# Performance work log

Measured on AMD Instinct MI355X. Metric: run time of the kernel, lower is better.

Reference implementation:

```python
import jax, jax.numpy as jnp
import numpy as np
from jax import lax

B, C, H, W = 8, 1, 1024, 1024


def _conv5(x, w, b):
    # x: [N, Cin, Hs, Ws], w: [1, Cin, 5, 5], b: [1]; 'same' padding (pad=2)
    return lax.conv_general_dilated(
        x, w, window_strides=(1, 1), padding=((2, 2), (2, 2)),
        dimension_numbers=("NCHW", "OIHW", "NCHW")) + b[None, :, None, None]


def _dir_scan(seq, pw, pb, cw, cb):
    # seq: [T, B, 1, Hs, Ws] slices in processing order.
    # s_0 = preconv(seq[0]); s_t = conv(cat(s_{t-1}, seq[t])).
    s0 = _conv5(seq[0], pw, pb)

    def step(carry, sl):
        s = _conv5(jnp.concatenate([carry, sl], axis=1), cw, cb)
        return s, s

    _, ys = lax.scan(step, s0, seq[1:])
    return jnp.concatenate([s0[None], ys], axis=0)  # [T, B, 1, Hs, Ws]


def setup_inputs() -> dict:
    key = jax.random.key(0)
    ks = jax.random.split(key, 17)
    inp = {"x": jax.random.normal(ks[0], (B, C, H, W), jnp.float32)}
    for i, name in enumerate(["pre1", "pre2", "pre3", "pre4"]):
        inp[name + "_w"] = jax.random.normal(ks[1 + 2 * i], (1, 1, 5, 5), jnp.float32) * 0.2
        inp[name + "_b"] = jax.random.normal(ks[2 + 2 * i], (1,), jnp.float32) * 0.1
    for i, name in enumerate(["c1", "c2", "c3", "c4"]):
        inp[name + "_w"] = jax.random.normal(ks[9 + 2 * i], (1, 2, 5, 5), jnp.float32) * 0.2
        inp[name + "_b"] = jax.random.normal(ks[10 + 2 * i], (1,), jnp.float32) * 0.1
    return inp


def reference(x, pre1_w, pre1_b, pre2_w, pre2_b, pre3_w, pre3_b, pre4_w, pre4_b,
              c1_w, c1_b, c2_w, c2_b, c3_w, c3_b, c4_w, c4_b):
    # Pass 1: top->down scan over rows h; conv spatial plane is (C, W).
    seq1 = jnp.transpose(x, (2, 0, 1, 3))[:, :, None]        # [H, B, 1, C, W]
    s1 = _dir_scan(seq1, pre1_w, pre1_b, c1_w, c1_b)          # states s_0..s_{H-1}
    # Pass 2: torch reads out1 channels H-1..0, i.e. s_0..s_{H-1} in order.
    s2 = _dir_scan(s1, pre2_w, pre2_b, c2_w, c2_b)            # states u_0..u_{H-1}
    # out2 (torch layout): channel j holds u_{H-1-j} -> [B, H, C, W]
    out2 = jnp.transpose(s2[::-1, :, 0], (1, 0, 2, 3))
    # Pass 3: left->right scan over w; conv spatial plane is (H, C).
    seq3 = jnp.transpose(out2, (3, 0, 1, 2))[:, :, None]      # [W, B, 1, H, C]
    s3 = _dir_scan(seq3, pre3_w, pre3_b, c3_w, c3_b)          # states v_0..v_{W-1}
    # Pass 4: torch reads out3 channels W-1..0, i.e. v_0..v_{W-1} in order.
    s4 = _dir_scan(s3, pre4_w, pre4_b, c4_w, c4_b)            # states z_0..z_{W-1}
    out4 = jnp.transpose(s4[::-1, :, 0], (1, 0, 2, 3))        # [B, W, H, C]
    return jnp.transpose(out4, (0, 3, 2, 1))                  # [B, C, H, W]
```

## Files before the change

### kernel.cpp

```cpp
#include <hip/hip_runtime.h>

#define HW 1024
#define NB 8
#define LPT 16
#define CHUNK 4
#define NCH (HW / CHUNK)
#define WARM 64

__device__ __forceinline__ float shfl_up1(float v)  { return __shfl_up(v, 1, 64); }
__device__ __forceinline__ float shfl_dn1(float v)  { return __shfl_down(v, 1, 64); }


#define LOADX(XD, T)                                                        \
    {                                                                       \
        const int tr_ = ((T) < HW) ? (T) : (HW - 1);                        \
        const float* rp_ = Ib + (size_t)tr_ * HW + base;                    \
        *(float4*)&XD[2]  = ((const float4*)rp_)[0];                        \
        *(float4*)&XD[6]  = ((const float4*)rp_)[1];                        \
        *(float4*)&XD[10] = ((const float4*)rp_)[2];                        \
        *(float4*)&XD[14] = ((const float4*)rp_)[3];                        \
    }

#define STEP(IS_PRE2, T, XC, XN, SC, SN, UC, UN)                            \
    {                                                                       \
        const int t_ = (T);                                                 \
        LOADX(XN, t_ + 2);                                                  \
        _Pragma("unroll")                                                   \
        for (int i = 0; i < 16; ++i) {                                      \
            float acc = cB1;                                                \
            _Pragma("unroll")                                               \
            for (int k = 0; k < 5; ++k) acc += A1[k] * SC[i + k];           \
            _Pragma("unroll")                                               \
            for (int k = 0; k < 5; ++k) acc += B1[k] * XC[i + k];           \
            SN[2 + i] = acc;                                                \
        }                                                                   \
        if (IS_PRE2) {                                                      \
            _Pragma("unroll")                                               \
            for (int i = 0; i < 16; ++i) {                                  \
                float acc = pB2;                                            \
                _Pragma("unroll")                                           \
                for (int k = 0; k < 5; ++k) acc += P2[k] * SC[i + k];       \
                UN[2 + i] = acc;                                            \
            }                                                               \
        } else {                                                            \
            _Pragma("unroll")                                               \
            for (int i = 0; i < 16; ++i) {                                  \
                float acc = cB2;                                            \
                _Pragma("unroll")                                           \
                for (int k = 0; k < 5; ++k) acc += A2[k] * UC[i + k];       \
                _Pragma("unroll")                                           \
                for (int k = 0; k < 5; ++k) acc += B2[k] * SC[i + k];       \
                UN[2 + i] = acc;                                            \
            }                                                               \
        }                                                                   \
              \
        float sa_ = shfl_up1(SN[16]), sb_ = shfl_up1(SN[17]);               \
        float sc_ = shfl_dn1(SN[2]),  sd_ = shfl_dn1(SN[3]);                \
        float ua_ = shfl_up1(UN[16]), ub_ = shfl_up1(UN[17]);               \
        float uc_ = shfl_dn1(UN[2]),  ud_ = shfl_dn1(UN[3]);                \
        float xa_ = shfl_up1(XN[16]), xb_ = shfl_up1(XN[17]);               \
        float xc_ = shfl_dn1(XN[2]),  xd_ = shfl_dn1(XN[3]);                \
        if (t_ >= T0) {       \
            _Pragma("unroll")                                               \
            for (int q = 0; q < 4; ++q) {                                   \
                float4 v_;                                                  \
                v_.x = UN[2 + 4 * q]; v_.y = UN[3 + 4 * q];                 \
                v_.z = UN[4 + 4 * q]; v_.w = UN[5 + 4 * q];                 \
                *(float4*)(Ob + (size_t)t_ * HW + base + 4 * q) = v_;       \
            }                                                               \
        }                                                                   \
        SN[0]  = lo ? 0.f : sa_; SN[1]  = lo ? 0.f : sb_;                   \
        SN[18] = hi ? 0.f : sc_; SN[19] = hi ? 0.f : sd_;                   \
        UN[0]  = lo ? 0.f : ua_; UN[1]  = lo ? 0.f : ub_;                   \
        UN[18] = hi ? 0.f : uc_; UN[19] = hi ? 0.f : ud_;                   \
        XN[0]  = lo ? 0.f : xa_; XN[1]  = lo ? 0.f : xb_;                   \
        XN[18] = hi ? 0.f : xc_; XN[19] = hi ? 0.f : xd_;                   \
    }

__global__ __launch_bounds__(64, 2) void scan_pair_wave(
    const float* __restrict__ I, float* __restrict__ O,
    const float* __restrict__ pw1, const float* __restrict__ pb1,
    const float* __restrict__ pw2, const float* __restrict__ pb2,
    const float* __restrict__ cw1, const float* __restrict__ cb1,
    const float* __restrict__ cw2, const float* __restrict__ cb2,
    int toff, int tstr)
{
    const int b     = blockIdx.x;
    const int chunk = blockIdx.y;
    const int T0 = chunk * CHUNK, T1 = T0 + CHUNK;
    const int g0 = (T0 - WARM > 0) ? (T0 - WARM) : 0;

    const int lane = threadIdx.x;
    const int base = lane * LPT;
    const bool lo = (lane == 0), hi = (lane == 63);

    float P1[5], P2[5], A1[5], B1[5], A2[5], B2[5];
#pragma unroll
    for (int k = 0; k < 5; ++k) {
        P1[k] = pw1[toff + k * tstr];
        P2[k] = pw2[toff + k * tstr];
        A1[k] = cw1[toff + k * tstr];
        B1[k] = cw1[25 + toff + k * tstr];
        A2[k] = cw2[toff + k * tstr];
        B2[k] = cw2[25 + toff + k * tstr];
    }
    const float pB1 = pb1[0], pB2 = pb2[0], cB1 = cb1[0], cB2 = cb2[0];

    const float* Ib = I + (size_t)b * HW * HW;
    float*       Ob = O + (size_t)b * HW * HW;

    float xeA[20], xeB[20], seA[20], seB[20], ueA[20], ueB[20];

#pragma unroll
    for (int i = 0; i < 20; ++i) ueA[i] = 0.f;

    LOADX(xeB, g0);
    LOADX(xeA, g0 + 1);
    {
        float a0 = shfl_up1(xeB[16]), a1 = shfl_up1(xeB[17]);
        float a2 = shfl_dn1(xeB[2]),  a3 = shfl_dn1(xeB[3]);
        float b0 = shfl_up1(xeA[16]), b1 = shfl_up1(xeA[17]);
        float b2 = shfl_dn1(xeA[2]),  b3 = shfl_dn1(xeA[3]);
        xeB[0]  = lo ? 0.f : a0; xeB[1]  = lo ? 0.f : a1;
        xeB[18] = hi ? 0.f : a2; xeB[19] = hi ? 0.f : a3;
        xeA[0]  = lo ? 0.f : b0; xeA[1]  = lo ? 0.f : b1;
        xeA[18] = hi ? 0.f : b2; xeA[19] = hi ? 0.f : b3;
    }
    if (g0 == 0) {
#pragma unroll
        for (int i = 0; i < 16; ++i) {
            float acc = pB1;
#pragma unroll
            for (int k = 0; k < 5; ++k) acc += P1[k] * xeB[i + k];
            seA[2 + i] = acc;
        }
    } else {
#pragma unroll
        for (int i = 0; i < 16; ++i) {
            float acc = cB1;
#pragma unroll
            for (int k = 0; k < 5; ++k) acc += B1[k] * xeB[i + k];
            seA[2 + i] = acc;
        }
    }
    {
        float sa = shfl_up1(seA[16]), sb = shfl_up1(seA[17]);
        float sc = shfl_dn1(seA[2]),  sd = shfl_dn1(seA[3]);
        seA[0]  = lo ? 0.f : sa; seA[1]  = lo ? 0.f : sb;
        seA[18] = hi ? 0.f : sc; seA[19] = hi ? 0.f : sd;
    }

    if (g0 == 0) {
        STEP(1, 0, xeA, xeB, seA, seB, ueA, ueB);
        for (int t = 1; t + 1 <= T1 - 2; t += 2) {
            STEP(0, t,     xeB, xeA, seB, seA, ueB, ueA);
            STEP(0, t + 1, xeA, xeB, seA, seB, ueA, ueB);
        }
    } else {
        int t = g0;
        for (; t + 1 <= T1 - 2; t += 2) {
            STEP(0, t,     xeA, xeB, seA, seB, ueA, ueB);
            STEP(0, t + 1, xeB, xeA, seB, seA, ueB, ueA);
        }
        STEP(0, T1 - 2, xeA, xeB, seA, seB, ueA, ueB);
    }

    {
        float un[16];
#pragma unroll
        for (int i = 0; i < 16; ++i) {
            float acc = cB2;
#pragma unroll
            for (int k = 0; k < 5; ++k) acc += A2[k] * ueB[i + k];
#pragma unroll
            for (int k = 0; k < 5; ++k) acc += B2[k] * seB[i + k];
            un[i] = acc;
        }
#pragma unroll
        for (int q = 0; q < 4; ++q) {
            float4 v;
            v.x = un[4 * q + 0]; v.y = un[4 * q + 1];
            v.z = un[4 * q + 2]; v.w = un[4 * q + 3];
            *(float4*)(Ob + (size_t)(T1 - 1) * HW + base + 4 * q) = v;
        }
    }
}

__global__ void transposeR_kernel(const float* __restrict__ in, float* __restrict__ out)
{
    __shared__ float tile[32][33];
    const int b  = blockIdx.z;
    const int r0 = blockIdx.y * 32;
    const int c0 = blockIdx.x * 32;
    const int tx = threadIdx.x, ty = threadIdx.y;
    const float* inb  = in  + (size_t)b * HW * HW;
    float*       outb = out + (size_t)b * HW * HW;

#pragma unroll
    for (int i = ty; i < 32; i += 8)
        tile[i][tx] = inb[(size_t)(HW - 1 - (r0 + i)) * HW + c0 + tx];
    __syncthreads();
#pragma unroll
    for (int i = ty; i < 32; i += 8)
        outb[(size_t)(c0 + i) * HW + r0 + tx] = tile[tx][i];
}

extern "C" void kernel_launch(void* const* d_in, const int* in_sizes, int n_in,
                              void* d_out, int out_size, void* d_ws, size_t ws_size,
                              hipStream_t stream)
{
    const float* x      = (const float*)d_in[0];
    const float* pre1_w = (const float*)d_in[1];
    const float* pre1_b = (const float*)d_in[2];
    const float* pre2_w = (const float*)d_in[3];
    const float* pre2_b = (const float*)d_in[4];
    const float* pre3_w = (const float*)d_in[5];
    const float* pre3_b = (const float*)d_in[6];
    const float* pre4_w = (const float*)d_in[7];
    const float* pre4_b = (const float*)d_in[8];
    const float* c1_w   = (const float*)d_in[9];
    const float* c1_b   = (const float*)d_in[10];
    const float* c2_w   = (const float*)d_in[11];
    const float* c2_b   = (const float*)d_in[12];
    const float* c3_w   = (const float*)d_in[13];
    const float* c3_b   = (const float*)d_in[14];
    const float* c4_w   = (const float*)d_in[15];
    const float* c4_b   = (const float*)d_in[16];

    float* out = (float*)d_out;
    float* ws  = (float*)d_ws;

    dim3 sg(NB, NCH), sb(64);
    dim3 tg(32, 32, NB), tb(32, 8);

    scan_pair_wave<<<sg, sb, 0, stream>>>(
        x, ws, pre1_w, pre1_b, pre2_w, pre2_b, c1_w, c1_b, c2_w, c2_b, 10, 1);

    transposeR_kernel<<<tg, tb, 0, stream>>>(ws, out);

    scan_pair_wave<<<sg, sb, 0, stream>>>(
        out, ws, pre3_w, pre3_b, pre4_w, pre4_b, c3_w, c3_b, c4_w, c4_b, 2, 5);

    transposeR_kernel<<<tg, tb, 0, stream>>>(ws, out);
}
```

Measured before the change: 204.5 us.

## Load x halos directly from memory, double chunk size, hoist state shuffles

Each lane now reads its two-element left and right halo of the input row straight from global memory instead of exchanging it through cross-lane shuffles. The halo is patched in at the start of the next step, which takes the shuffles off the critical path. The state shuffles move to just after the state is computed so they overlap with the second conv. The time chunk per block doubles, which halves the redundant warm-up recomputation relative to useful work but also halves the number of blocks. Launch bounds drop to one block per SIMD, which allows more registers.

```diff
diff --git a/kernel.cpp b/kernel.cpp
--- a/kernel.cpp
+++ b/kernel.cpp
@@ -3,7 +3,7 @@
 #define HW 1024
 #define NB 8
 #define LPT 16
-#define CHUNK 4
+#define CHUNK 8
 #define NCH (HW / CHUNK)
 #define WARM 64
 
@@ -11,7 +11,7 @@
 __device__ __forceinline__ float shfl_dn1(float v)  { return __shfl_down(v, 1, 64); }
 
 
-#define LOADX(XD, T)                                                        \
+#define LOADX(XD, XL, XR, T)                                                \
     {                                                                       \
         const int tr_ = ((T) < HW) ? (T) : (HW - 1);                        \
         const float* rp_ = Ib + (size_t)tr_ * HW + base;                    \
@@ -19,12 +19,22 @@
         *(float4*)&XD[6]  = ((const float4*)rp_)[1];                        \
         *(float4*)&XD[10] = ((const float4*)rp_)[2];                        \
         *(float4*)&XD[14] = ((const float4*)rp_)[3];                        \
-    }
-
-#define STEP(IS_PRE2, T, XC, XN, SC, SN, UC, UN)                            \
+        XL = *(const float2*)(lo ? rp_ : rp_ - 2);          \
+        XR = *(const float2*)(hi ? rp_ : rp_ + 16);        \
+    }
+
+#define FINX(XC, XL, XR)                                                    \
+    {                                                                       \
+        XC[0]  = lo ? 0.f : XL.x;  XC[1]  = lo ? 0.f : XL.y;                \
+        XC[18] = hi ? 0.f : XR.x;  XC[19] = hi ? 0.f : XR.y;                \
+    }
+
+#define STEP(IS_PRE2, T, XC, XCL, XCR, XN, XNL, XNR, SC, SN, UC, UN)        \
     {                                                                       \
         const int t_ = (T);                                                 \
-        LOADX(XN, t_ + 2);                                                  \
+        FINX(XC, XCL, XCR);      \
+        LOADX(XN, XNL, XNR, t_ + 2);     \
+                           \
         _Pragma("unroll")                                                   \
         for (int i = 0; i < 16; ++i) {                                      \
             float acc = cB1;                                                \
@@ -34,6 +44,10 @@
             for (int k = 0; k < 5; ++k) acc += B1[k] * XC[i + k];           \
             SN[2 + i] = acc;                                                \
         }                                                                   \
+                  \
+        float sa_ = shfl_up1(SN[16]), sb_ = shfl_up1(SN[17]);               \
+        float sc_ = shfl_dn1(SN[2]),  sd_ = shfl_dn1(SN[3]);                \
+         \
         if (IS_PRE2) {                                                      \
             _Pragma("unroll")                                               \
             for (int i = 0; i < 16; ++i) {                                  \
@@ -53,14 +67,10 @@
                 UN[2 + i] = acc;                                            \
             }                                                               \
         }                                                                   \
-              \
-        float sa_ = shfl_up1(SN[16]), sb_ = shfl_up1(SN[17]);               \
-        float sc_ = shfl_dn1(SN[2]),  sd_ = shfl_dn1(SN[3]);                \
+                              \
         float ua_ = shfl_up1(UN[16]), ub_ = shfl_up1(UN[17]);               \
         float uc_ = shfl_dn1(UN[2]),  ud_ = shfl_dn1(UN[3]);                \
-        float xa_ = shfl_up1(XN[16]), xb_ = shfl_up1(XN[17]);               \
-        float xc_ = shfl_dn1(XN[2]),  xd_ = shfl_dn1(XN[3]);                \
-        if (t_ >= T0) {       \
+        if (t_ >= T0) {                                                     \
             _Pragma("unroll")                                               \
             for (int q = 0; q < 4; ++q) {                                   \
                 float4 v_;                                                  \
@@ -73,11 +83,9 @@
         SN[18] = hi ? 0.f : sc_; SN[19] = hi ? 0.f : sd_;                   \
         UN[0]  = lo ? 0.f : ua_; UN[1]  = lo ? 0.f : ub_;                   \
         UN[18] = hi ? 0.f : uc_; UN[19] = hi ? 0.f : ud_;                   \
-        XN[0]  = lo ? 0.f : xa_; XN[1]  = lo ? 0.f : xb_;                   \
-        XN[18] = hi ? 0.f : xc_; XN[19] = hi ? 0.f : xd_;                   \
-    }
-
-__global__ __launch_bounds__(64, 2) void scan_pair_wave(
+    }
+
+__global__ __launch_bounds__(64, 1) void scan_pair_wave(
     const float* __restrict__ I, float* __restrict__ O,
     const float* __restrict__ pw1, const float* __restrict__ pb1,
     const float* __restrict__ pw2, const float* __restrict__ pb2,
@@ -110,22 +118,14 @@
     float*       Ob = O + (size_t)b * HW * HW;
 
     float xeA[20], xeB[20], seA[20], seB[20], ueA[20], ueB[20];
+    float2 xlA, xrA, xlB, xrB;
 
 #pragma unroll
     for (int i = 0; i < 20; ++i) ueA[i] = 0.f;
 
-    LOADX(xeB, g0);
-    LOADX(xeA, g0 + 1);
-    {
-        float a0 = shfl_up1(xeB[16]), a1 = shfl_up1(xeB[17]);
-        float a2 = shfl_dn1(xeB[2]),  a3 = shfl_dn1(xeB[3]);
-        float b0 = shfl_up1(xeA[16]), b1 = shfl_up1(xeA[17]);
-        float b2 = shfl_dn1(xeA[2]),  b3 = shfl_dn1(xeA[3]);
-        xeB[0]  = lo ? 0.f : a0; xeB[1]  = lo ? 0.f : a1;
-        xeB[18] = hi ? 0.f : a2; xeB[19] = hi ? 0.f : a3;
-        xeA[0]  = lo ? 0.f : b0; xeA[1]  = lo ? 0.f : b1;
-        xeA[18] = hi ? 0.f : b2; xeA[19] = hi ? 0.f : b3;
-    }
+    LOADX(xeB, xlB, xrB, g0);
+    LOADX(xeA, xlA, xrA, g0 + 1);
+    FINX(xeB, xlB, xrB);
     if (g0 == 0) {
 #pragma unroll
         for (int i = 0; i < 16; ++i) {
@@ -151,18 +151,18 @@
     }
 
     if (g0 == 0) {
-        STEP(1, 0, xeA, xeB, seA, seB, ueA, ueB);
+        STEP(1, 0, xeA, xlA, xrA, xeB, xlB, xrB, seA, seB, ueA, ueB);
         for (int t = 1; t + 1 <= T1 - 2; t += 2) {
-            STEP(0, t,     xeB, xeA, seB, seA, ueB, ueA);
-            STEP(0, t + 1, xeA, xeB, seA, seB, ueA, ueB);
+            STEP(0, t,     xeB, xlB, xrB, xeA, xlA, xrA, seB, seA, ueB, ueA);
+            STEP(0, t + 1, xeA, xlA, xrA, xeB, xlB, xrB, seA, seB, ueA, ueB);
         }
     } else {
         int t = g0;
         for (; t + 1 <= T1 - 2; t += 2) {
-            STEP(0, t,     xeA, xeB, seA, seB, ueA, ueB);
-            STEP(0, t + 1, xeB, xeA, seB, seA, ueB, ueA);
-        }
-        STEP(0, T1 - 2, xeA, xeB, seA, seB, ueA, ueB);
+            STEP(0, t,     xeA, xlA, xrA, xeB, xlB, xrB, seA, seB, ueA, ueB);
+            STEP(0, t + 1, xeB, xlB, xrB, xeA, xlA, xrA, seB, seA, ueB, ueA);
+        }
+        STEP(0, T1 - 2, xeA, xlA, xrA, xeB, xlB, xrB, seA, seB, ueA, ueB);
     }
 
     {
```

New measurement: 190.2 us. 1.08x faster.

## Use DPP wave shifts for halo exchange and double chunk length

Applied to the files above, without the earlier changes.

Replaces the ds-based __shfl_up/__shfl_down halo exchanges with DPP wave_shr/wave_shl moves. Bound_ctrl zero-fill now supplies the boundary zeros, so the lane==0/lane==63 selects are removed. The input halo exchange moves to just before each use, and each state is exchanged right after it is computed. CHUNK goes from 4 to 8, which halves the redundant 64-step warm-up recomputation per output row, at the cost of half as many blocks. Launch bounds are relaxed to one block per SIMD. The wave-level DPP shift controls are a GFX9-specific encoding, which adds a portability risk.

```diff
diff --git a/kernel.cpp b/kernel.cpp
--- a/kernel.cpp
+++ b/kernel.cpp
@@ -3,12 +3,18 @@
 #define HW 1024
 #define NB 8
 #define LPT 16
-#define CHUNK 4
+#define CHUNK 8
 #define NCH (HW / CHUNK)
 #define WARM 64
 
-__device__ __forceinline__ float shfl_up1(float v)  { return __shfl_up(v, 1, 64); }
-__device__ __forceinline__ float shfl_dn1(float v)  { return __shfl_down(v, 1, 64); }
+__device__ __forceinline__ float dpp_up1(float v) {
+    return __int_as_float(__builtin_amdgcn_update_dpp(
+        0, __float_as_int(v), 0x138, 0xf, 0xf, true));
+}
+__device__ __forceinline__ float dpp_dn1(float v) {
+    return __int_as_float(__builtin_amdgcn_update_dpp(
+        0, __float_as_int(v), 0x130, 0xf, 0xf, true));
+}
 
 
 #define LOADX(XD, T)                                                        \
@@ -24,7 +30,11 @@
 #define STEP(IS_PRE2, T, XC, XN, SC, SN, UC, UN)                            \
     {                                                                       \
         const int t_ = (T);                                                 \
-        LOADX(XN, t_ + 2);                                                  \
+                     \
+        XC[0]  = dpp_up1(XC[16]); XC[1]  = dpp_up1(XC[17]);                 \
+        XC[18] = dpp_dn1(XC[2]);  XC[19] = dpp_dn1(XC[3]);                  \
+        LOADX(XN, t_ + 2);              \
+                           \
         _Pragma("unroll")                                                   \
         for (int i = 0; i < 16; ++i) {                                      \
             float acc = cB1;                                                \
@@ -34,6 +44,9 @@
             for (int k = 0; k < 5; ++k) acc += B1[k] * XC[i + k];           \
             SN[2 + i] = acc;                                                \
         }                                                                   \
+        SN[0]  = dpp_up1(SN[16]); SN[1]  = dpp_up1(SN[17]);                 \
+        SN[18] = dpp_dn1(SN[2]);  SN[19] = dpp_dn1(SN[3]);                  \
+         \
         if (IS_PRE2) {                                                      \
             _Pragma("unroll")                                               \
             for (int i = 0; i < 16; ++i) {                                  \
@@ -53,14 +66,9 @@
                 UN[2 + i] = acc;                                            \
             }                                                               \
         }                                                                   \
-              \
-        float sa_ = shfl_up1(SN[16]), sb_ = shfl_up1(SN[17]);               \
-        float sc_ = shfl_dn1(SN[2]),  sd_ = shfl_dn1(SN[3]);                \
-        float ua_ = shfl_up1(UN[16]), ub_ = shfl_up1(UN[17]);               \
-        float uc_ = shfl_dn1(UN[2]),  ud_ = shfl_dn1(UN[3]);                \
-        float xa_ = shfl_up1(XN[16]), xb_ = shfl_up1(XN[17]);               \
-        float xc_ = shfl_dn1(XN[2]),  xd_ = shfl_dn1(XN[3]);                \
-        if (t_ >= T0) {       \
+        UN[0]  = dpp_up1(UN[16]); UN[1]  = dpp_up1(UN[17]);                 \
+        UN[18] = dpp_dn1(UN[2]);  UN[19] = dpp_dn1(UN[3]);                  \
+        if (t_ >= T0) {                                                     \
             _Pragma("unroll")                                               \
             for (int q = 0; q < 4; ++q) {                                   \
                 float4 v_;                                                  \
@@ -69,15 +77,9 @@
                 *(float4*)(Ob + (size_t)t_ * HW + base + 4 * q) = v_;       \
             }                                                               \
         }                                                                   \
-        SN[0]  = lo ? 0.f : sa_; SN[1]  = lo ? 0.f : sb_;                   \
-        SN[18] = hi ? 0.f : sc_; SN[19] = hi ? 0.f : sd_;                   \
-        UN[0]  = lo ? 0.f : ua_; UN[1]  = lo ? 0.f : ub_;                   \
-        UN[18] = hi ? 0.f : uc_; UN[19] = hi ? 0.f : ud_;                   \
-        XN[0]  = lo ? 0.f : xa_; XN[1]  = lo ? 0.f : xb_;                   \
-        XN[18] = hi ? 0.f : xc_; XN[19] = hi ? 0.f : xd_;                   \
-    }
-
-__global__ __launch_bounds__(64, 2) void scan_pair_wave(
+    }
+
+__global__ __launch_bounds__(64, 1) void scan_pair_wave(
     const float* __restrict__ I, float* __restrict__ O,
     const float* __restrict__ pw1, const float* __restrict__ pb1,
     const float* __restrict__ pw2, const float* __restrict__ pb2,
@@ -92,7 +94,6 @@
 
     const int lane = threadIdx.x;
     const int base = lane * LPT;
-    const bool lo = (lane == 0), hi = (lane == 63);
 
     float P1[5], P2[5], A1[5], B1[5], A2[5], B2[5];
 #pragma unroll
@@ -116,16 +117,8 @@
 
     LOADX(xeB, g0);
     LOADX(xeA, g0 + 1);
-    {
-        float a0 = shfl_up1(xeB[16]), a1 = shfl_up1(xeB[17]);
-        float a2 = shfl_dn1(xeB[2]),  a3 = shfl_dn1(xeB[3]);
-        float b0 = shfl_up1(xeA[16]), b1 = shfl_up1(xeA[17]);
-        float b2 = shfl_dn1(xeA[2]),  b3 = shfl_dn1(xeA[3]);
-        xeB[0]  = lo ? 0.f : a0; xeB[1]  = lo ? 0.f : a1;
-        xeB[18] = hi ? 0.f : a2; xeB[19] = hi ? 0.f : a3;
-        xeA[0]  = lo ? 0.f : b0; xeA[1]  = lo ? 0.f : b1;
-        xeA[18] = hi ? 0.f : b2; xeA[19] = hi ? 0.f : b3;
-    }
+    xeB[0]  = dpp_up1(xeB[16]); xeB[1]  = dpp_up1(xeB[17]);
+    xeB[18] = dpp_dn1(xeB[2]);  xeB[19] = dpp_dn1(xeB[3]);
     if (g0 == 0) {
 #pragma unroll
         for (int i = 0; i < 16; ++i) {
@@ -143,12 +136,8 @@
             seA[2 + i] = acc;
         }
     }
-    {
-        float sa = shfl_up1(seA[16]), sb = shfl_up1(seA[17]);
-        float sc = shfl_dn1(seA[2]),  sd = shfl_dn1(seA[3]);
-        seA[0]  = lo ? 0.f : sa; seA[1]  = lo ? 0.f : sb;
-        seA[18] = hi ? 0.f : sc; seA[19] = hi ? 0.f : sd;
-    }
+    seA[0]  = dpp_up1(seA[16]); seA[1]  = dpp_up1(seA[17]);
+    seA[18] = dpp_dn1(seA[2]);  seA[19] = dpp_dn1(seA[3]);
 
     if (g0 == 0) {
         STEP(1, 0, xeA, xeB, seA, seB, ueA, ueB);
```

New measurement: 186.7 us. 8.7% less time.
